# Performance work log

Measured on AMD Instinct MI355X. Metric: run time of the kernel, lower is better.

## Reference

```python
import jax, jax.numpy as jnp
import numpy as np

D_SPEC, D_PRE, D_CTX, D_H = 552, 256, 128, 1024


def _lstm_cell(x, h, c, Wih, Whh, bih, bhh):
    # PyTorch gate order: i, f, g, o
    g = x @ Wih.T + bih + h @ Whh.T + bhh
    i, f, gg, o = jnp.split(g, 4, axis=-1)
    c_new = jax.nn.sigmoid(f) * c + jax.nn.sigmoid(i) * jnp.tanh(gg)
    h_new = jax.nn.sigmoid(o) * jnp.tanh(c_new)
    return h_new, c_new


def _conv1d(x, w, b):
    # x: [B, C_in, L], w: [C_out, C_in, K], 'same' padding for K=5
    y = jax.lax.conv_general_dilated(x, w, window_strides=(1,), padding=[(2, 2)],
                                     dimension_numbers=('NCH', 'OIH', 'NCH'))
    return y + b[None, :, None]


def setup_inputs() -> dict:
    key = jax.random.key(0)
    ks = jax.random.split(key, 26)
    s = 0.05
    shapes = {
        'S_pad': (600, 64, D_SPEC),
        'pre_W1': (D_PRE, D_SPEC), 'pre_b1': (D_PRE,),
        'pre_W2': (D_PRE, D_PRE), 'pre_b2': (D_PRE,),
        'Wih0': (4 * D_H, D_PRE + D_CTX), 'Whh0': (4 * D_H, D_H),
        'bih0': (4 * D_H,), 'bhh0': (4 * D_H,),
        'Wih1': (4 * D_H, D_H), 'Whh1': (4 * D_H, D_H),
        'bih1': (4 * D_H,), 'bhh1': (4 * D_H,),
        'lin_W': (D_SPEC, D_H + D_CTX), 'lin_b': (D_SPEC,),
        'cw1': (512, D_SPEC, 5), 'cb1': (512,),
        'cw2': (512, 512, 5), 'cb2': (512,),
        'cw3': (512, 512, 5), 'cb3': (512,),
        'cw4': (512, 512, 5), 'cb4': (512,),
        'cw5': (D_SPEC, 512, 5), 'cb5': (D_SPEC,),
    }
    out = {}
    for i, (name, shp) in enumerate(shapes.items()):
        scale = 1.0 if name == 'S_pad' else s
        out[name] = scale * jax.random.normal(ks[i], shp, dtype=jnp.float32)
    return out


def reference(S_pad, pre_W1, pre_b1, pre_W2, pre_b2,
              Wih0, Whh0, bih0, bhh0, Wih1, Whh1, bih1, bhh1,
              lin_W, lin_b, cw1, cb1, cw2, cb2, cw3, cb3, cw4, cb4, cw5, cb5):
    L, B, _ = S_pad.shape
    # teacher forcing: input frame at t is S_pad[t-1] (zeros at t=0) -> precompute pre_net batched
    in_frames = jnp.concatenate([jnp.zeros((1, B, D_SPEC), S_pad.dtype), S_pad[:-1]], axis=0)
    pre = jax.nn.relu(in_frames @ pre_W1.T + pre_b1)
    pre = jax.nn.relu(pre @ pre_W2.T + pre_b2)  # dropout = identity (eval)
    ctx = jnp.zeros((L, B, D_CTX), S_pad.dtype)  # dummy_context
    lstm_in = jnp.concatenate([pre, ctx], axis=-1)  # [L, B, 384]

    h0 = jnp.zeros((B, D_H), S_pad.dtype)
    init = (h0, h0, h0, h0)  # (h0, c0, h1, c1)

    def step(carry, x):
        h0, c0, h1, c1 = carry
        h0, c0 = _lstm_cell(x, h0, c0, Wih0, Whh0, bih0, bhh0)
        h1, c1 = _lstm_cell(h0, h1, c1, Wih1, Whh1, bih1, bhh1)
        return (h0, c0, h1, c1), h1

    _, outs = jax.lax.scan(step, init, lstm_in)  # [L, B, 1024]
    S_pred = jnp.concatenate([outs, ctx], axis=-1) @ lin_W.T + lin_b  # [L, B, 552]

    x = jnp.transpose(S_pred, (1, 2, 0))  # [B, 552, L]
    x = jnp.tanh(_conv1d(x, cw1, cb1))
    x = jnp.tanh(_conv1d(x, cw2, cb2))
    x = jnp.tanh(_conv1d(x, cw3, cb3))
    x = jnp.tanh(_conv1d(x, cw4, cb4))
    x = _conv1d(x, cw5, cb5)
    S_residual = jnp.transpose(x, (2, 0, 1))  # [L, B, 552]
    return S_pred + S_residual
```

## Files before the change

kernel.cpp:

```cpp
#include <hip/hip_runtime.h>
#include <cstdint>
#include <cstddef>

typedef __bf16 bf16;
typedef __attribute__((ext_vector_type(8))) __bf16 bf16x8;
typedef __attribute__((ext_vector_type(4))) float f32x4;
typedef __attribute__((ext_vector_type(4))) unsigned u32x4;

#define DEV static __device__ __forceinline__

DEV float sigm_(float x) { return 1.f / (1.f + __expf(-x)); }
DEV float tanhf_(float x) {
  float e = __expf(-2.f * fabsf(x));
  float t = (1.f - e) / (1.f + e);
  return x < 0.f ? -t : t;
}

DEV void gload_lds16(const bf16* g, bf16* l) {
  __builtin_amdgcn_global_load_lds((const __attribute__((address_space(1))) void*)g,
                                   (__attribute__((address_space(3))) void*)l, 16, 0, 0);
}

__global__ void k_frames(const float* __restrict__ S, bf16* __restrict__ dst) {
  int idx = blockIdx.x * 256 + threadIdx.x;
  if (idx >= 38400 * 576) return;
  int r = idx / 576, c = idx - r * 576;
  int t = r >> 6, b = r & 63;
  float v = (t == 0 || c >= 552) ? 0.f : S[((size_t)(t - 1) * 64 + b) * 552 + c];
  dst[idx] = (bf16)v;
}

__global__ void k_pad2d(const float* __restrict__ src, bf16* __restrict__ dst,
                        int N, int Cdst, int Csrc, int Rsrc, int sstride) {
  int idx = blockIdx.x * 256 + threadIdx.x;
  if (idx >= N) return;
  int r = idx / Cdst, c = idx - r * Cdst;
  float v = (r < Rsrc && c < Csrc) ? src[(size_t)r * sstride + c] : 0.f;
  dst[idx] = (bf16)v;
}

__global__ void k_w0c(const float* __restrict__ Whh0, const float* __restrict__ Wih0,
                      bf16* __restrict__ dst) {
  int idx = blockIdx.x * 256 + threadIdx.x;
  if (idx >= 4096 * 1280) return;
  int r = idx / 1280, k = idx - r * 1280;
  float v = (k < 1024) ? Whh0[(size_t)r * 1024 + k] : Wih0[(size_t)r * 384 + (k - 1024)];
  dst[idx] = (bf16)v;
}

__global__ void k_w1c(const float* __restrict__ Wih1, const float* __restrict__ Whh1,
                      bf16* __restrict__ dst) {
  int idx = blockIdx.x * 256 + threadIdx.x;
  if (idx >= 4096 * 2048) return;
  int r = idx / 2048, k = idx - r * 2048;
  float v = (k < 1024) ? Wih1[(size_t)r * 1024 + k] : Whh1[(size_t)r * 1024 + (k - 1024)];
  dst[idx] = (bf16)v;
}

__global__ void k_convw(const float* __restrict__ src, bf16* __restrict__ dst,
                        int N, int Cpad, int Cisrc, int Cosrc) {
  int idx = blockIdx.x * 256 + threadIdx.x;
  if (idx >= N) return;
  int per = 5 * Cpad;
  int co = idx / per, rem = idx - co * per;
  int tap = rem / Cpad, ci = rem - tap * Cpad;
  float v = (co < Cosrc && ci < Cisrc) ? src[((size_t)co * Cisrc + ci) * 5 + tap] : 0.f;
  dst[idx] = (bf16)v;
}

__global__ void k_zpad(bf16* __restrict__ X0, bf16* __restrict__ X1, bf16* __restrict__ X2) {
  int idx = blockIdx.x * 256 + threadIdx.x;
  if (idx >= 64 * 4 * 1600) return;
  int per = 4 * 1600;
  int b = idx / per, rem = idx - b * per;
  int rr = rem / 1600, c = rem - rr * 1600;
  int row = (rr < 2) ? rr : 600 + rr;
  if (c < 576) X0[((size_t)b * 604 + row) * 576 + c] = (bf16)0.f;
  else if (c < 1088) X1[((size_t)b * 604 + row) * 512 + (c - 576)] = (bf16)0.f;
  else X2[((size_t)b * 604 + row) * 512 + (c - 1088)] = (bf16)0.f;
}

enum { M_RELU = 0, M_LINEAR = 1, M_CONVT = 2, M_CONVF = 3 };

template <int MODE>
__global__ __launch_bounds__(256) void gemm_k(
    const bf16* __restrict__ A, const bf16* __restrict__ B, int Ktot, int Kstride,
    int Brows, const float* __restrict__ bias,
    bf16* __restrict__ outB, int outStride, int colP, int colOff,
    float* __restrict__ outF, bf16* __restrict__ outX) {
  const int tid = threadIdx.x;
  const int lane = tid & 63, wv = tid >> 6;
  const int n0 = blockIdx.x * 128, m0 = blockIdx.y * 128;
  const int bz = blockIdx.z;
  __shared__ bf16 As[128 * 64];
  __shared__ bf16 Bs[128 * 64];
  f32x4 acc[4][4] = {};
  const int wr = wv >> 1, wc = wv & 1;
  int tap = 0, ci0 = 0;

  for (int kb = 0; kb < Ktot; kb += 64) {
#pragma unroll
    for (int j = 0; j < 4; ++j) {
      int rt = wv * 32 + j * 8 + (lane >> 3);
      const bf16* gp;
      if (MODE == M_CONVT || MODE == M_CONVF) {
        int l = m0 + rt;
        if (l > 599) l = 599;
        gp = A + ((size_t)(bz * 604 + l + tap)) * Kstride + ci0 + (lane & 7) * 8;
      } else {
        gp = A + (size_t)(m0 + rt) * Kstride + kb + (lane & 7) * 8;
      }
      gload_lds16(gp, &As[(wv * 32 + j * 8) * 64]);
    }
#pragma unroll
    for (int j = 0; j < 4; ++j) {
      int rn = n0 + wv * 32 + j * 8 + (lane >> 3);
      if (rn >= Brows) rn = Brows - 1;
      const bf16* gp = B + (size_t)rn * Ktot + kb + (lane & 7) * 8;
      gload_lds16(gp, &Bs[(wv * 32 + j * 8) * 64]);
    }
    __syncthreads();
#pragma unroll
    for (int ks = 0; ks < 2; ++ks) {
      const int ko = ks * 32 + (lane >> 4) * 8;
      bf16x8 af[4], bfr[4];
#pragma unroll
      for (int i = 0; i < 4; ++i) {
        af[i] = *(const bf16x8*)&As[(wr * 64 + i * 16 + (lane & 15)) * 64 + ko];
        bfr[i] = *(const bf16x8*)&Bs[(wc * 64 + i * 16 + (lane & 15)) * 64 + ko];
      }
#pragma unroll
      for (int mi = 0; mi < 4; ++mi)
#pragma unroll
        for (int ni = 0; ni < 4; ++ni)
          acc[mi][ni] = __builtin_amdgcn_mfma_f32_16x16x32_bf16(af[mi], bfr[ni], acc[mi][ni], 0, 0, 0);
    }
    __syncthreads();
    ci0 += 64;
    if (ci0 == Kstride) { ci0 = 0; ++tap; }
  }

  const int r0 = (lane >> 4) * 4, cc = lane & 15;
#pragma unroll
  for (int mi = 0; mi < 4; ++mi) {
#pragma unroll
    for (int ni = 0; ni < 4; ++ni) {
#pragma unroll
      for (int r = 0; r < 4; ++r) {
        float v = acc[mi][ni][r];
        int gr = m0 + wr * 64 + mi * 16 + r0 + r;
        int gc = n0 + wc * 64 + ni * 16 + cc;
        if (MODE == M_RELU) {
          v += bias[gc];
          v = fmaxf(v, 0.f);
          outB[(size_t)(gr >> 6) * outStride + (size_t)(gr & 63) * colP + colOff + gc] = (bf16)v;
        } else if (MODE == M_LINEAR) {
          if (gc < 552) {
            v += bias[gc];
            int t = gr >> 6, b = gr & 63;
            outF[(size_t)gr * 552 + gc] = v;
            outX[((size_t)b * 604 + t + 2) * 576 + gc] = (bf16)v;
          }
        } else if (MODE == M_CONVT) {
          if (gr < 600) {
            v = tanhf_(v + bias[gc]);
            outB[((size_t)bz * 604 + gr + 2) * 512 + gc] = (bf16)v;
          }
        } else {
          if (gr < 600 && gc < 552) {
            v += bias[gc];
            float* p = outF + ((size_t)gr * 64 + bz) * 552 + gc;
            *p += v;
          }
        }
      }
    }
  }
}

template <int LAYER>
DEV void scan_impl(bf16* __restrict__ C0, bf16* __restrict__ H1,
                   const bf16* __restrict__ W, const float* __restrict__ bi,
                   const float* __restrict__ bh, unsigned* __restrict__ flags,
                   float* gb, int u0, int b0, int mh, int ub) {
  constexpr int KT = LAYER ? 2048 : 1280;
  constexpr int NKS = KT / 256;
  const int tid = threadIdx.x, lane = tid & 63, w = tid >> 6;
  const int kb = w * (KT / 8);

  bf16x8 wreg[4][NKS];
#pragma unroll
  for (int gi = 0; gi < 4; ++gi)
#pragma unroll
    for (int ks = 0; ks < NKS; ++ks)
      wreg[gi][ks] = *(const bf16x8*)(W + (size_t)(gi * 1024 + u0 + (lane & 15)) * KT +
                                      kb + ks * 32 + (lane >> 4) * 8);

  const int uc = tid & 15, bl = tid >> 4;
  float bs[4];
#pragma unroll
  for (int g = 0; g < 4; ++g) bs[g] = bi[g * 1024 + u0 + uc] + bh[g * 1024 + u0 + uc];
  float cst = 0.f;
  const int rotc = (bl + 4 * uc) & 31;

  unsigned* flO = flags + (LAYER * 2 + mh) * 64 * 32;
  unsigned* flP = flags + mh * 64 * 32;

  const unsigned* fl;
  int fb, nf, thrAdd;
  if (!LAYER) {
    fl = flO; fb = w * 10; nf = (w < 6) ? 10 : (w == 6 ? 4 : 0); thrAdd = 0;
  } else if (w < 4) {
    fl = flP; fb = w * 16; nf = 16; thrAdd = 1;
  } else {
    fl = flO; fb = (w - 4) * 16; nf = 16; thrAdd = 0;
  }

  const int r0 = lane & 15, q8 = (lane >> 4) * 8;
  const int un = lane & 15, qb = (lane >> 4) * 4;

  for (int t = 0; t < 600; ++t) {
    if (nf && (LAYER || t > 0)) {
      const unsigned thr = (unsigned)(t + thrAdd);
      for (;;) {
        unsigned f = (lane < nf)
            ? __hip_atomic_load(&fl[(fb + lane) << 5], __ATOMIC_RELAXED, __HIP_MEMORY_SCOPE_AGENT)
            : 0xFFFFFFFFu;
        if (!__ballot(f < thr)) break;
        __builtin_amdgcn_s_sleep(1);
      }
      __builtin_amdgcn_sched_barrier(0);
      asm volatile("" ::: "memory");
    }

    const bf16* A0;
    int RS;
    if (!LAYER) {
      RS = 1280;
      A0 = C0 + (size_t)t * 81920 + (size_t)(b0 + r0) * 1280 + kb + q8;
    } else if (w < 4) {
      RS = 1280;
      A0 = C0 + (size_t)(t + 1) * 81920 + (size_t)(b0 + r0) * 1280 + kb + q8;
    } else {
      RS = 1024;
      A0 = H1 + (size_t)(t + 1) * 65536 + (size_t)(b0 + r0) * 1024 + (kb - 1024) + q8;
    }
    const bf16* A1 = A0 + 16 * RS;

    f32x4 acc[4][2] = {};
#pragma unroll
    for (int ks = 0; ks < NKS; ++ks) {
      bf16x8 a0 = *(const bf16x8*)(A0 + ks * 32);
      bf16x8 a1 = *(const bf16x8*)(A1 + ks * 32);
#pragma unroll
      for (int gi = 0; gi < 4; ++gi) {
        acc[gi][0] = __builtin_amdgcn_mfma_f32_16x16x32_bf16(a0, wreg[gi][ks], acc[gi][0], 0, 0, 0);
        acc[gi][1] = __builtin_amdgcn_mfma_f32_16x16x32_bf16(a1, wreg[gi][ks], acc[gi][1], 0, 0, 0);
      }
    }

#pragma unroll
    for (int gi = 0; gi < 4; ++gi)
#pragma unroll
      for (int b2 = 0; b2 < 2; ++b2)
        *(f32x4*)&gb[((w * 4 + gi) * 16 + un) * 32 + ((b2 * 16 + qb + 4 * un) & 31)] = acc[gi][b2];

    asm volatile("s_waitcnt lgkmcnt(0)" ::: "memory");
    __builtin_amdgcn_s_barrier();
    __builtin_amdgcn_sched_barrier(0);

    float s4[4];
#pragma unroll
    for (int g = 0; g < 4; ++g) {
      float a = 0.f;
#pragma unroll
      for (int ww = 0; ww < 8; ++ww) a += gb[((ww * 4 + g) * 16 + uc) * 32 + rotc];
      s4[g] = a + bs[g];
    }
    float c = sigm_(s4[1]) * cst + sigm_(s4[0]) * tanhf_(s4[2]);
    cst = c;
    float h = sigm_(s4[3]) * tanhf_(c);

    float h1 = __shfl_down(h, 1), h2 = __shfl_down(h, 2), h3 = __shfl_down(h, 3);
    if ((uc & 3) == 0) {
      union { bf16 q[4]; unsigned long long u; } pk;
      pk.q[0] = (bf16)h; pk.q[1] = (bf16)h1; pk.q[2] = (bf16)h2; pk.q[3] = (bf16)h3;
      unsigned long long* dst = LAYER
          ? (unsigned long long*)(H1 + (size_t)(t + 2) * 65536 + (size_t)(b0 + bl) * 1024 + u0 + uc)
          : (unsigned long long*)(C0 + (size_t)(t + 1) * 81920 + (size_t)(b0 + bl) * 1280 + u0 + uc);
      __hip_atomic_store(dst, pk.u, __ATOMIC_RELAXED, __HIP_MEMORY_SCOPE_AGENT);
    }
    asm volatile("s_waitcnt vmcnt(0)" ::: "memory");
    __builtin_amdgcn_s_barrier();
    __builtin_amdgcn_sched_barrier(0);
    if (tid == 0)
      __hip_atomic_store(&flO[ub << 5], (unsigned)(t + 1), __ATOMIC_RELAXED, __HIP_MEMORY_SCOPE_AGENT);
  }
}

__global__ __launch_bounds__(512, 1) void lstm_k(
    bf16* __restrict__ C0, bf16* __restrict__ H1,
    const bf16* __restrict__ W0, const bf16* __restrict__ W1,
    const float* __restrict__ bi0, const float* __restrict__ bh0,
    const float* __restrict__ bi1, const float* __restrict__ bh1,
    unsigned* __restrict__ flags) {
  __shared__ float gb[512 * 32];
  const int bid = blockIdx.x;
  const int layer = bid >> 7, sub = bid & 127;
  const int mh = sub >> 6, ub = sub & 63;
  const int u0 = ub * 16, b0 = mh * 32;
  if (layer == 0)
    scan_impl<0>(C0, H1, W0, bi0, bh0, flags, gb, u0, b0, mh, ub);
  else
    scan_impl<1>(C0, H1, W1, bi1, bh1, flags, gb, u0, b0, mh, ub);
}

static inline unsigned gdiv(size_t n) { return (unsigned)((n + 255) / 256); }

extern "C" void kernel_launch(void* const* d_in, const int* in_sizes, int n_in,
                              void* d_out, int out_size, void* d_ws, size_t ws_size,
                              hipStream_t stream) {
  const float* S = (const float*)d_in[0];
  const float* preW1 = (const float*)d_in[1];
  const float* preb1 = (const float*)d_in[2];
  const float* preW2 = (const float*)d_in[3];
  const float* preb2 = (const float*)d_in[4];
  const float* Wih0 = (const float*)d_in[5];
  const float* Whh0 = (const float*)d_in[6];
  const float* bih0 = (const float*)d_in[7];
  const float* bhh0 = (const float*)d_in[8];
  const float* Wih1 = (const float*)d_in[9];
  const float* Whh1 = (const float*)d_in[10];
  const float* bih1 = (const float*)d_in[11];
  const float* bhh1 = (const float*)d_in[12];
  const float* linW = (const float*)d_in[13];
  const float* linb = (const float*)d_in[14];
  const float* cw1 = (const float*)d_in[15];
  const float* cb1 = (const float*)d_in[16];
  const float* cw2 = (const float*)d_in[17];
  const float* cb2 = (const float*)d_in[18];
  const float* cw3 = (const float*)d_in[19];
  const float* cb3 = (const float*)d_in[20];
  const float* cw4 = (const float*)d_in[21];
  const float* cb4 = (const float*)d_in[22];
  const float* cw5 = (const float*)d_in[23];
  const float* cb5 = (const float*)d_in[24];
  float* out = (float*)d_out;

  char* ws = (char*)d_ws;
  size_t off = 0;
  auto alloc = [&](size_t bytes) -> char* {
    char* p = ws + off;
    off += (bytes + 255) & ~(size_t)255;
    return p;
  };
  unsigned* flags = (unsigned*)alloc(32768);
  bf16* H1 = (bf16*)alloc(602ull * 64 * 1024 * 2);
  bf16* frames = (bf16*)alloc(38400ull * 576 * 2);
  bf16* pre1 = (bf16*)alloc(38400ull * 256 * 2);
  bf16* W0c = (bf16*)alloc(4096ull * 1280 * 2);
  bf16* W1c = (bf16*)alloc(4096ull * 2048 * 2);
  bf16* pW1b = (bf16*)alloc(256ull * 576 * 2);
  bf16* pW2b = (bf16*)alloc(256ull * 256 * 2);
  bf16* linWb = (bf16*)alloc(576ull * 1024 * 2);
  bf16* c1r = (bf16*)alloc(512ull * 5 * 576 * 2);
  bf16* c2r = (bf16*)alloc(512ull * 5 * 512 * 2);
  bf16* c3r = (bf16*)alloc(512ull * 5 * 512 * 2);
  bf16* c4r = (bf16*)alloc(512ull * 5 * 512 * 2);
  bf16* c5r = (bf16*)alloc(576ull * 5 * 512 * 2);
  bf16* X0 = (bf16*)alloc(64ull * 604 * 576 * 2);
  bf16* X1 = (bf16*)alloc(64ull * 604 * 512 * 2);
  bf16* X2 = (bf16*)alloc(64ull * 604 * 512 * 2);
  bf16* C0 = X0;

  hipMemsetAsync(ws, 0, 32768 + 2ull * 64 * 1024 * 2, stream);
  hipMemsetAsync(C0, 0, 64ull * 1280 * 2, stream);

  k_frames<<<gdiv(38400ull * 576), 256, 0, stream>>>(S, frames);
  k_pad2d<<<gdiv(256 * 576), 256, 0, stream>>>(preW1, pW1b, 256 * 576, 576, 552, 256, 552);
  k_pad2d<<<gdiv(256 * 256), 256, 0, stream>>>(preW2, pW2b, 256 * 256, 256, 256, 256, 256);
  k_pad2d<<<gdiv(576 * 1024), 256, 0, stream>>>(linW, linWb, 576 * 1024, 1024, 1024, 552, 1152);
  k_w0c<<<gdiv(4096ull * 1280), 256, 0, stream>>>(Whh0, Wih0, W0c);
  k_w1c<<<gdiv(4096ull * 2048), 256, 0, stream>>>(Wih1, Whh1, W1c);
  k_convw<<<gdiv(512ull * 5 * 576), 256, 0, stream>>>(cw1, c1r, 512 * 5 * 576, 576, 552, 512);
  k_convw<<<gdiv(512ull * 5 * 512), 256, 0, stream>>>(cw2, c2r, 512 * 5 * 512, 512, 512, 512);
  k_convw<<<gdiv(512ull * 5 * 512), 256, 0, stream>>>(cw3, c3r, 512 * 5 * 512, 512, 512, 512);
  k_convw<<<gdiv(512ull * 5 * 512), 256, 0, stream>>>(cw4, c4r, 512 * 5 * 512, 512, 512, 512);
  k_convw<<<gdiv(576ull * 5 * 512), 256, 0, stream>>>(cw5, c5r, 576 * 5 * 512, 512, 512, 552);

  gemm_k<M_RELU><<<dim3(2, 300, 1), 256, 0, stream>>>(frames, pW1b, 576, 576, 256, preb1,
                                                      pre1, 16384, 256, 0, nullptr, nullptr);
  gemm_k<M_RELU><<<dim3(2, 300, 1), 256, 0, stream>>>(pre1, pW2b, 256, 256, 256, preb2,
                                                      C0, 81920, 1280, 1024, nullptr, nullptr);
  lstm_k<<<dim3(256), 512, 0, stream>>>(C0, H1, W0c, W1c, bih0, bhh0, bih1, bhh1, flags);
  k_zpad<<<gdiv(64 * 4 * 1600), 256, 0, stream>>>(X0, X1, X2);
  gemm_k<M_LINEAR><<<dim3(5, 300, 1), 256, 0, stream>>>(H1 + 131072, linWb, 1024, 1024, 576, linb,
                                                        nullptr, 0, 0, 0, out, X0);
  gemm_k<M_CONVT><<<dim3(4, 5, 64), 256, 0, stream>>>(X0, c1r, 2880, 576, 512, cb1,
                                                      X1, 0, 0, 0, nullptr, nullptr);
  gemm_k<M_CONVT><<<dim3(4, 5, 64), 256, 0, stream>>>(X1, c2r, 2560, 512, 512, cb2,
                                                      X2, 0, 0, 0, nullptr, nullptr);
  gemm_k<M_CONVT><<<dim3(4, 5, 64), 256, 0, stream>>>(X2, c3r, 2560, 512, 512, cb3,
                                                      X1, 0, 0, 0, nullptr, nullptr);
  gemm_k<M_CONVT><<<dim3(4, 5, 64), 256, 0, stream>>>(X1, c4r, 2560, 512, 512, cb4,
                                                      X2, 0, 0, 0, nullptr, nullptr);
  gemm_k<M_CONVF><<<dim3(5, 5, 64), 256, 0, stream>>>(X2, c5r, 2560, 512, 576, cb5,
                                                      nullptr, 0, 0, 0, out, nullptr);
  (void)in_sizes; (void)n_in; (void)out_size; (void)ws_size;
}
```

Measured before the change: 4.978 ms.

## Double-buffer LDS tiles in GEMM to overlap global loads with MFMA

Turns the shared GEMM/conv kernel's single LDS tile into two buffers. The next K-tile is issued via global_load_lds before computing the current one, with an explicit vmcnt wait so only the current tile's loads must finish. This hides global-load latency behind MFMA work. It doubles LDS use per block to 64KB, which may reduce occupancy, and relies on hand-placed waitcnt and barriers being correct.

```diff
diff --git a/kernel.cpp b/kernel.cpp
--- a/kernel.cpp
+++ b/kernel.cpp
@@ -5,7 +5,6 @@
 typedef __bf16 bf16;
 typedef __attribute__((ext_vector_type(8))) __bf16 bf16x8;
 typedef __attribute__((ext_vector_type(4))) float f32x4;
-typedef __attribute__((ext_vector_type(4))) unsigned u32x4;
 
 #define DEV static __device__ __forceinline__
 
@@ -92,13 +91,14 @@
   const int lane = tid & 63, wv = tid >> 6;
   const int n0 = blockIdx.x * 128, m0 = blockIdx.y * 128;
   const int bz = blockIdx.z;
-  __shared__ bf16 As[128 * 64];
-  __shared__ bf16 Bs[128 * 64];
+  __shared__ bf16 As[2][128 * 64];
+  __shared__ bf16 Bs[2][128 * 64];
   f32x4 acc[4][4] = {};
   const int wr = wv >> 1, wc = wv & 1;
-  int tap = 0, ci0 = 0;
-
-  for (int kb = 0; kb < Ktot; kb += 64) {
+  const int nt = Ktot >> 6;
+  int tapS = 0, ci0S = 0;
+
+  auto stage = [&](int buf, int kb) {
 #pragma unroll
     for (int j = 0; j < 4; ++j) {
       int rt = wv * 32 + j * 8 + (lane >> 3);
@@ -106,28 +106,47 @@
       if (MODE == M_CONVT || MODE == M_CONVF) {
         int l = m0 + rt;
         if (l > 599) l = 599;
-        gp = A + ((size_t)(bz * 604 + l + tap)) * Kstride + ci0 + (lane & 7) * 8;
+        gp = A + ((size_t)(bz * 604 + l + tapS)) * Kstride + ci0S + (lane & 7) * 8;
       } else {
         gp = A + (size_t)(m0 + rt) * Kstride + kb + (lane & 7) * 8;
       }
-      gload_lds16(gp, &As[(wv * 32 + j * 8) * 64]);
+      gload_lds16(gp, &As[buf][(wv * 32 + j * 8) * 64]);
     }
 #pragma unroll
     for (int j = 0; j < 4; ++j) {
       int rn = n0 + wv * 32 + j * 8 + (lane >> 3);
       if (rn >= Brows) rn = Brows - 1;
       const bf16* gp = B + (size_t)rn * Ktot + kb + (lane & 7) * 8;
-      gload_lds16(gp, &Bs[(wv * 32 + j * 8) * 64]);
-    }
-    __syncthreads();
+      gload_lds16(gp, &Bs[buf][(wv * 32 + j * 8) * 64]);
+    }
+    if (MODE == M_CONVT || MODE == M_CONVF) {
+      ci0S += 64;
+      if (ci0S == Kstride) { ci0S = 0; ++tapS; }
+    }
+  };
+
+  stage(0, 0);
+
+  for (int i = 0; i < nt; ++i) {
+    if (i + 1 < nt) {
+      stage((i + 1) & 1, (i + 1) << 6);
+      asm volatile("s_waitcnt vmcnt(8)" ::: "memory");
+    } else {
+      asm volatile("s_waitcnt vmcnt(0)" ::: "memory");
+    }
+    __builtin_amdgcn_sched_barrier(0);
+    __builtin_amdgcn_s_barrier();
+
+    const bf16* Ab = &As[i & 1][0];
+    const bf16* Bb = &Bs[i & 1][0];
 #pragma unroll
     for (int ks = 0; ks < 2; ++ks) {
       const int ko = ks * 32 + (lane >> 4) * 8;
       bf16x8 af[4], bfr[4];
 #pragma unroll
-      for (int i = 0; i < 4; ++i) {
-        af[i] = *(const bf16x8*)&As[(wr * 64 + i * 16 + (lane & 15)) * 64 + ko];
-        bfr[i] = *(const bf16x8*)&Bs[(wc * 64 + i * 16 + (lane & 15)) * 64 + ko];
+      for (int j = 0; j < 4; ++j) {
+        af[j] = *(const bf16x8*)&Ab[(wr * 64 + j * 16 + (lane & 15)) * 64 + ko];
+        bfr[j] = *(const bf16x8*)&Bb[(wc * 64 + j * 16 + (lane & 15)) * 64 + ko];
       }
 #pragma unroll
       for (int mi = 0; mi < 4; ++mi)
@@ -135,9 +154,7 @@
         for (int ni = 0; ni < 4; ++ni)
           acc[mi][ni] = __builtin_amdgcn_mfma_f32_16x16x32_bf16(af[mi], bfr[ni], acc[mi][ni], 0, 0, 0);
     }
-    __syncthreads();
-    ci0 += 64;
-    if (ci0 == Kstride) { ci0 = 0; ++tap; }
+    __builtin_amdgcn_s_barrier();
   }
 
   const int r0 = (lane >> 4) * 4, cc = lane & 15;
```

After: 5.107 ms. +2.6%, slower.
